# Kernel optimization log

Hardware: AMD Instinct MI355X
Metric: run time of the kernel (lower is better)

The kernel has to match this reference:

```python
import jax, jax.numpy as jnp
import numpy as np

BLOCK = 32          # per_1x32 microscaling block size along K
FP4_MAX = 6.0       # largest magnitude representable in e2m1
FP4_EMAX = 2.0      # exponent of largest fp4 binade (4..6)


def _quant_dequant_mxfp4(x):
    """Simulate MXFP4 (e2m1 elements, shared power-of-two E8M0 scale per 1x32
    block along the last dim): quantize then dequantize. x: [..., K], K % 32 == 0."""
    shape = x.shape
    xb = x.reshape(*shape[:-1], shape[-1] // BLOCK, BLOCK)
    amax = jnp.max(jnp.abs(xb), axis=-1, keepdims=True)
    # shared scale: 2^(floor(log2(amax)) - emax) so the block max lands in the top binade
    exp = jnp.floor(jnp.log2(jnp.maximum(amax, jnp.finfo(x.dtype).tiny))) - FP4_EMAX
    scale = jnp.where(amax > 0, jnp.exp2(exp), jnp.ones_like(amax))
    q = jnp.clip(xb / scale, -FP4_MAX, FP4_MAX)
    aq = jnp.abs(q)
    # e2m1 ulp: 0.5 on [0,2), 1 on [2,4), 2 on [4,6]
    lsb = jnp.where(aq < 2.0, 0.5, jnp.where(aq < 4.0, 1.0, 2.0))
    qr = jnp.round(q / lsb) * lsb  # round-to-nearest-even onto the fp4 grid
    return (qr * scale).reshape(shape)


def setup_inputs() -> dict:
    key = jax.random.key(0)
    k1, k2, k3 = jax.random.split(key, 3)
    B, S, K, N = 4, 2048, 2048, 2048
    inp = jax.random.normal(k1, (B, S, K), dtype=jnp.float32)
    weight = jax.random.normal(k2, (N, K), dtype=jnp.float32) * (1.0 / np.sqrt(K))
    bias = jax.random.normal(k3, (N,), dtype=jnp.float32) * 0.02
    return {"input": inp, "weight": weight, "bias": bias}


def reference(input, weight, bias):
    # both activation and weight are fake-quantized to MXFP4 per 1x32 blocks
    # along the contraction (in_features) dim, then a standard GEMM + bias.
    orig_shape = input.shape
    a = _quant_dequant_mxfp4(input.reshape(-1, orig_shape[-1]))  # [M, K]
    w = _quant_dequant_mxfp4(weight)                              # [N, K]
    out = jnp.einsum("mk,nk->mn", a, w) + bias
    return out.reshape(*orig_shape[:-1], weight.shape[0])
```

## Files before the change

### kernel.cpp

```cpp
#include <hip/hip_runtime.h>
#include <cstdint>


#define BM 128
#define BN 128
#define BK 128
#define NBUF 2

typedef float floatx4 __attribute__((ext_vector_type(4)));
typedef int intx8 __attribute__((ext_vector_type(8)));

#define GLOBAL_AS __attribute__((address_space(1)))
#define LDS_AS __attribute__((address_space(3)))


__device__ __forceinline__ int enc1(float x, float inv) {
    float q = x * inv;
    q = fminf(fmaxf(q, -6.0f), 6.0f);
    int s = (int)(__float_as_uint(q) >> 31) << 3;
    float aq = fabsf(q);
    float ilsb = aq < 2.0f ? 2.0f : (aq < 4.0f ? 1.0f : 0.5f);
    float lsb  = aq < 2.0f ? 0.5f : (aq < 4.0f ? 1.0f : 2.0f);
    float ar = rintf(aq * ilsb) * lsb;
    int c;
    if (ar < 2.0f)      c = (int)(ar * 2.0f);
    else if (ar < 4.0f) c = 2 + (int)ar;
    else                c = 4 + (int)(ar * 0.5f);
    return c | s;
}

__global__ void quant_mxfp4_v3(const float* __restrict__ A, uint8_t* __restrict__ Aq,
                               uint8_t* __restrict__ Asc,
                               const float* __restrict__ W, uint8_t* __restrict__ Wq,
                               uint8_t* __restrict__ Wsc,
                               long na4, long ntot4) {
    long t = (long)blockIdx.x * 256 + threadIdx.x;
    if (t >= ntot4) return;
    const float* src; uint8_t* dq; uint8_t* ds; long idx;
    if (t < na4) { src = A; dq = Aq; ds = Asc; idx = t; }
    else         { src = W; dq = Wq; ds = Wsc; idx = t - na4; }

    float4 f = ((const float4*)src)[idx];
    float amax = fmaxf(fmaxf(fabsf(f.x), fabsf(f.y)),
                       fmaxf(fabsf(f.z), fabsf(f.w)));
    amax = fmaxf(amax, __shfl_xor(amax, 1));
    amax = fmaxf(amax, __shfl_xor(amax, 2));
    amax = fmaxf(amax, __shfl_xor(amax, 4));

    int ebits = (int)((__float_as_uint(amax) >> 23) & 0xff);
    int sb;
    float inv;
    if (amax > 0.0f) {
        sb = ebits - 2; if (sb < 0) sb = 0;
        inv = __uint_as_float((unsigned)((256 - ebits) & 255) << 23);
    } else {
        sb = 127;
        inv = 0.0f;
    }

    int c0 = enc1(f.x, inv), c1 = enc1(f.y, inv);
    int c2 = enc1(f.z, inv), c3 = enc1(f.w, inv);
    ((unsigned short*)dq)[idx] =
        (unsigned short)(c0 | (c1 << 4) | (c2 << 8) | (c3 << 12));
    if ((idx & 7) == 0) ds[idx >> 3] = (uint8_t)sb;
}


__global__ __launch_bounds__(256, 3) void gemm_fp4_pipe(
        const uint8_t* __restrict__ Aq, const uint8_t* __restrict__ Asc,
        const uint8_t* __restrict__ Wq, const uint8_t* __restrict__ Wsc,
        const float* __restrict__ bias, float* __restrict__ C,
        int M, int N, int K) {
    __shared__ __align__(16) uint8_t sA[NBUF][BM * BK / 2];
    __shared__ __align__(16) uint8_t sB[NBUF][BN * BK / 2];
    __shared__ __align__(16) uint8_t sSA[NBUF][BM * 4];
    __shared__ __align__(16) uint8_t sSB[NBUF][BN * 4];

    const int tid = threadIdx.x;
    const int lane = tid & 63;
    const int w = tid >> 6;
    const int wr = w >> 1;
    const int wc = w & 1;
    const int row16 = lane & 15;
    const int quad = lane >> 4;
    const int shq = quad * 8;

    const int id = blockIdx.x;
    const int g = id & 7, h = id >> 3;
    const int by = g + 8 * (h & 7);
    const int bx = h >> 3;
    const int m0 = by * BM;
    const int n0 = bx * BN;
    const int KB2 = K >> 1, KB32 = K >> 5;
    const int NT = K / BK;

    const int fragoff = (quad ^ ((row16 ^ (row16 >> 2)) & 3)) * 16;
    const int rA = wr * 64 + row16;
    const int rB = wc * 64 + row16;

    floatx4 acc[4][4];
#pragma unroll
    for (int i = 0; i < 4; i++)
#pragma unroll
        for (int j = 0; j < 4; j++) acc[i][j] = (floatx4){0.f, 0.f, 0.f, 0.f};

    auto stage = [&](int tt) {
        const int bb = tt & 1;
        const int kb = tt * (BK / 2);
#pragma unroll
        for (int it = 0; it < 2; ++it) {
            int idx = it * 256 + tid;
            int row = idx >> 2, c = idx & 3;
            int gsw = c ^ ((row ^ (row >> 2)) & 3);
            const uint8_t* src = Aq + (size_t)(m0 + row) * KB2 + kb + gsw * 16;
            __builtin_amdgcn_global_load_lds((GLOBAL_AS void*)src,
                (LDS_AS void*)(&sA[bb][idx * 16]), 16, 0, 0);
        }
#pragma unroll
        for (int it = 0; it < 2; ++it) {
            int idx = it * 256 + tid;
            int row = idx >> 2, c = idx & 3;
            int gsw = c ^ ((row ^ (row >> 2)) & 3);
            const uint8_t* src = Wq + (size_t)(n0 + row) * KB2 + kb + gsw * 16;
            __builtin_amdgcn_global_load_lds((GLOBAL_AS void*)src,
                (LDS_AS void*)(&sB[bb][idx * 16]), 16, 0, 0);
        }
        if (tid < 128) {
            const uint8_t* src = Asc + (size_t)(m0 + tid) * KB32 + tt * 4;
            __builtin_amdgcn_global_load_lds((GLOBAL_AS void*)src,
                (LDS_AS void*)(&sSA[bb][tid * 4]), 4, 0, 0);
        } else {
            const uint8_t* src = Wsc + (size_t)(n0 + tid - 128) * KB32 + tt * 4;
            __builtin_amdgcn_global_load_lds((GLOBAL_AS void*)src,
                (LDS_AS void*)(&sSB[bb][(tid - 128) * 4]), 4, 0, 0);
        }
    };

    stage(0);
    if (NT > 1) stage(1);
    if (NT > 1) asm volatile("s_waitcnt vmcnt(5)" ::: "memory");
    else        asm volatile("s_waitcnt vmcnt(0)" ::: "memory");
    __builtin_amdgcn_sched_barrier(0);
    __builtin_amdgcn_s_barrier();
    __builtin_amdgcn_sched_barrier(0);

    for (int t = 0; t < NT; ++t) {
        const int p = t & 1;
        const uint8_t* pa = sA[p];
        const uint8_t* pb = sB[p];

        intx8 A8[4], B8[4];
        int sab[4], swb[4];
#pragma unroll
        for (int ni = 0; ni < 4; ++ni) {
            int r = rB + ni * 16;
            int4 f = *(const int4*)(pb + r * 64 + fragoff);
            B8[ni] = (intx8){f.x, f.y, f.z, f.w, 0, 0, 0, 0};
            swb[ni] = (*(const int*)(&sSB[p][r * 4]) >> shq) & 0xff;
        }
#pragma unroll
        for (int mi = 0; mi < 4; ++mi) {
            int r = rA + mi * 16;
            int4 f = *(const int4*)(pa + r * 64 + fragoff);
            A8[mi] = (intx8){f.x, f.y, f.z, f.w, 0, 0, 0, 0};
            sab[mi] = (*(const int*)(&sSA[p][r * 4]) >> shq) & 0xff;
        }

        asm volatile("s_waitcnt lgkmcnt(0)" ::: "memory");
        __builtin_amdgcn_sched_barrier(0);
        __builtin_amdgcn_s_barrier();
        __builtin_amdgcn_sched_barrier(0);

        if (t + 2 < NT) stage(t + 2);

        __builtin_amdgcn_s_setprio(1);
#pragma unroll
        for (int mi = 0; mi < 4; ++mi) {
#pragma unroll
            for (int ni = 0; ni < 4; ++ni) {
                acc[mi][ni] = __builtin_amdgcn_mfma_scale_f32_16x16x128_f8f6f4(
                    A8[mi], B8[ni], acc[mi][ni], 4, 4, 0, sab[mi], 0, swb[ni]);
            }
        }
        __builtin_amdgcn_s_setprio(0);

        if (t < NT - 1) {
            if (t + 2 < NT) asm volatile("s_waitcnt vmcnt(5)" ::: "memory");
            else            asm volatile("s_waitcnt vmcnt(0)" ::: "memory");
            __builtin_amdgcn_sched_barrier(0);
            __builtin_amdgcn_s_barrier();
            __builtin_amdgcn_sched_barrier(0);
        }
    }

#pragma unroll
    for (int ni = 0; ni < 4; ++ni) {
        int n = n0 + wc * 64 + ni * 16 + row16;
        float bv = bias[n];
#pragma unroll
        for (int mi = 0; mi < 4; ++mi) {
            int mbase = m0 + wr * 64 + mi * 16 + quad * 4;
#pragma unroll
            for (int r = 0; r < 4; ++r) {
                C[(size_t)(mbase + r) * N + n] = acc[mi][ni][r] + bv;
            }
        }
    }
}


extern "C" void kernel_launch(void* const* d_in, const int* in_sizes, int n_in,
                              void* d_out, int out_size, void* d_ws, size_t ws_size,
                              hipStream_t stream) {
    const float* inp  = (const float*)d_in[0];
    const float* wgt  = (const float*)d_in[1];
    const float* bias = (const float*)d_in[2];
    float* out = (float*)d_out;

    const int N = in_sizes[2];
    const int K = in_sizes[1] / N;
    const long M = (long)in_sizes[0] / K;

    uint8_t* Aq4 = (uint8_t*)d_ws;
    uint8_t* Wq4 = Aq4 + (size_t)M * K / 2;
    uint8_t* Asc = Wq4 + (size_t)N * K / 2;
    uint8_t* Wsc = Asc + (size_t)M * K / 32;

    long na4   = (long)M * K / 4;
    long ntot4 = na4 + (long)N * K / 4;
    quant_mxfp4_v3<<<dim3((ntot4 + 255) / 256), dim3(256), 0, stream>>>(
        inp, Aq4, Asc, wgt, Wq4, Wsc, na4, ntot4);

    dim3 grid((N / BN) * (int)(M / BM));
    gemm_fp4_pipe<<<grid, dim3(256), 0, stream>>>(
        Aq4, Asc, Wq4, Wsc, bias, out, (int)M, N, K);
}
```

Before: 160.2 us.

## Transpose MX scale layout, drop LDS swizzle, raise occupancy to 4 waves

```diff
diff --git a/kernel.cpp b/kernel.cpp
--- a/kernel.cpp
+++ b/kernel.cpp
@@ -5,7 +5,6 @@
 #define BM 128
 #define BN 128
 #define BK 128
-#define NBUF 2
 
 typedef float floatx4 __attribute__((ext_vector_type(4)));
 typedef int intx8 __attribute__((ext_vector_type(8)));
@@ -29,16 +28,16 @@
     return c | s;
 }
 
-__global__ void quant_mxfp4_v3(const float* __restrict__ A, uint8_t* __restrict__ Aq,
-                               uint8_t* __restrict__ Asc,
+__global__ void quant_mxfp4_v4(const float* __restrict__ A, uint8_t* __restrict__ Aq,
+                               uint8_t* __restrict__ AscT,
                                const float* __restrict__ W, uint8_t* __restrict__ Wq,
-                               uint8_t* __restrict__ Wsc,
-                               long na4, long ntot4) {
+                               uint8_t* __restrict__ WscT,
+                               long na4, long ntot4, int s4, long Mr, long Nr) {
     long t = (long)blockIdx.x * 256 + threadIdx.x;
     if (t >= ntot4) return;
-    const float* src; uint8_t* dq; uint8_t* ds; long idx;
-    if (t < na4) { src = A; dq = Aq; ds = Asc; idx = t; }
-    else         { src = W; dq = Wq; ds = Wsc; idx = t - na4; }
+    const float* src; uint8_t* dq; uint8_t* ds; long idx; long rows;
+    if (t < na4) { src = A; dq = Aq; ds = AscT; idx = t; rows = Mr; }
+    else         { src = W; dq = Wq; ds = WscT; idx = t - na4; rows = Nr; }
 
     float4 f = ((const float4*)src)[idx];
     float amax = fmaxf(fmaxf(fabsf(f.x), fabsf(f.y)),
@@ -62,19 +61,23 @@
     int c2 = enc1(f.z, inv), c3 = enc1(f.w, inv);
     ((unsigned short*)dq)[idx] =
         (unsigned short)(c0 | (c1 << 4) | (c2 << 8) | (c3 << 12));
-    if ((idx & 7) == 0) ds[idx >> 3] = (uint8_t)sb;
-}
-
-
-__global__ __launch_bounds__(256, 3) void gemm_fp4_pipe(
-        const uint8_t* __restrict__ Aq, const uint8_t* __restrict__ Asc,
-        const uint8_t* __restrict__ Wq, const uint8_t* __restrict__ Wsc,
+    if ((idx & 7) == 0) {
+        long m  = idx >> s4;
+        int  kb = (int)((idx & ((1L << s4) - 1)) >> 3);
+        ds[(size_t)kb * rows + m] = (uint8_t)sb;
+    }
+}
+
+
+__global__ __launch_bounds__(256, 4) void gemm_fp4_v4(
+        const uint8_t* __restrict__ Aq, const uint8_t* __restrict__ AscT,
+        const uint8_t* __restrict__ Wq, const uint8_t* __restrict__ WscT,
         const float* __restrict__ bias, float* __restrict__ C,
         int M, int N, int K) {
-    __shared__ __align__(16) uint8_t sA[NBUF][BM * BK / 2];
-    __shared__ __align__(16) uint8_t sB[NBUF][BN * BK / 2];
-    __shared__ __align__(16) uint8_t sSA[NBUF][BM * 4];
-    __shared__ __align__(16) uint8_t sSB[NBUF][BN * 4];
+    __shared__ __align__(16) uint8_t sA[2][BM * 64];
+    __shared__ __align__(16) uint8_t sB[2][BN * 64];
+    __shared__ __align__(16) uint8_t sSA[2][4 * 128];
+    __shared__ __align__(16) uint8_t sSB[2][4 * 128];
 
     const int tid = threadIdx.x;
     const int lane = tid & 63;
@@ -83,7 +86,6 @@
     const int wc = w & 1;
     const int row16 = lane & 15;
     const int quad = lane >> 4;
-    const int shq = quad * 8;
 
     const int id = blockIdx.x;
     const int g = id & 7, h = id >> 3;
@@ -91,10 +93,9 @@
     const int bx = h >> 3;
     const int m0 = by * BM;
     const int n0 = bx * BN;
-    const int KB2 = K >> 1, KB32 = K >> 5;
+    const int KB2 = K >> 1;
     const int NT = K / BK;
 
-    const int fragoff = (quad ^ ((row16 ^ (row16 >> 2)) & 3)) * 16;
     const int rA = wr * 64 + row16;
     const int rB = wc * 64 + row16;
 
@@ -106,13 +107,12 @@
 
     auto stage = [&](int tt) {
         const int bb = tt & 1;
-        const int kb = tt * (BK / 2);
+        const int kb = tt * 64;
 #pragma unroll
         for (int it = 0; it < 2; ++it) {
             int idx = it * 256 + tid;
             int row = idx >> 2, c = idx & 3;
-            int gsw = c ^ ((row ^ (row >> 2)) & 3);
-            const uint8_t* src = Aq + (size_t)(m0 + row) * KB2 + kb + gsw * 16;
+            const uint8_t* src = Aq + (size_t)(m0 + row) * KB2 + kb + c * 16;
             __builtin_amdgcn_global_load_lds((GLOBAL_AS void*)src,
                 (LDS_AS void*)(&sA[bb][idx * 16]), 16, 0, 0);
         }
@@ -120,66 +120,65 @@
         for (int it = 0; it < 2; ++it) {
             int idx = it * 256 + tid;
             int row = idx >> 2, c = idx & 3;
-            int gsw = c ^ ((row ^ (row >> 2)) & 3);
-            const uint8_t* src = Wq + (size_t)(n0 + row) * KB2 + kb + gsw * 16;
+            const uint8_t* src = Wq + (size_t)(n0 + row) * KB2 + kb + c * 16;
             __builtin_amdgcn_global_load_lds((GLOBAL_AS void*)src,
                 (LDS_AS void*)(&sB[bb][idx * 16]), 16, 0, 0);
         }
         if (tid < 128) {
-            const uint8_t* src = Asc + (size_t)(m0 + tid) * KB32 + tt * 4;
+            int kbi = tid >> 5, moff = (tid & 31) * 4;
+            const uint8_t* src = AscT + (size_t)(4 * tt + kbi) * M + m0 + moff;
             __builtin_amdgcn_global_load_lds((GLOBAL_AS void*)src,
                 (LDS_AS void*)(&sSA[bb][tid * 4]), 4, 0, 0);
         } else {
-            const uint8_t* src = Wsc + (size_t)(n0 + tid - 128) * KB32 + tt * 4;
-            __builtin_amdgcn_global_load_lds((GLOBAL_AS void*)src,
-                (LDS_AS void*)(&sSB[bb][(tid - 128) * 4]), 4, 0, 0);
+            int tw = tid - 128;
+            int kbi = tw >> 5, noff = (tw & 31) * 4;
+            const uint8_t* src = WscT + (size_t)(4 * tt + kbi) * N + n0 + noff;
+            __builtin_amdgcn_global_load_lds((GLOBAL_AS void*)src,
+                (LDS_AS void*)(&sSB[bb][tw * 4]), 4, 0, 0);
         }
     };
 
     stage(0);
-    if (NT > 1) stage(1);
-    if (NT > 1) asm volatile("s_waitcnt vmcnt(5)" ::: "memory");
-    else        asm volatile("s_waitcnt vmcnt(0)" ::: "memory");
+    stage(1);
+    asm volatile("s_waitcnt vmcnt(5)" ::: "memory");
     __builtin_amdgcn_sched_barrier(0);
     __builtin_amdgcn_s_barrier();
-    __builtin_amdgcn_sched_barrier(0);
 
     for (int t = 0; t < NT; ++t) {
         const int p = t & 1;
         const uint8_t* pa = sA[p];
         const uint8_t* pb = sB[p];
 
-        intx8 A8[4], B8[4];
+        int4 afr[4], bfr[4];
         int sab[4], swb[4];
 #pragma unroll
         for (int ni = 0; ni < 4; ++ni) {
             int r = rB + ni * 16;
-            int4 f = *(const int4*)(pb + r * 64 + fragoff);
-            B8[ni] = (intx8){f.x, f.y, f.z, f.w, 0, 0, 0, 0};
-            swb[ni] = (*(const int*)(&sSB[p][r * 4]) >> shq) & 0xff;
+            bfr[ni] = *(const int4*)(pb + r * 64 + quad * 16);
+            swb[ni] = (int)sSB[p][quad * 128 + wc * 64 + ni * 16 + row16];
         }
 #pragma unroll
         for (int mi = 0; mi < 4; ++mi) {
             int r = rA + mi * 16;
-            int4 f = *(const int4*)(pa + r * 64 + fragoff);
-            A8[mi] = (intx8){f.x, f.y, f.z, f.w, 0, 0, 0, 0};
-            sab[mi] = (*(const int*)(&sSA[p][r * 4]) >> shq) & 0xff;
+            afr[mi] = *(const int4*)(pa + r * 64 + quad * 16);
+            sab[mi] = (int)sSA[p][quad * 128 + wr * 64 + mi * 16 + row16];
         }
 
         asm volatile("s_waitcnt lgkmcnt(0)" ::: "memory");
         __builtin_amdgcn_sched_barrier(0);
         __builtin_amdgcn_s_barrier();
-        __builtin_amdgcn_sched_barrier(0);
 
         if (t + 2 < NT) stage(t + 2);
 
         __builtin_amdgcn_s_setprio(1);
 #pragma unroll
         for (int mi = 0; mi < 4; ++mi) {
+            intx8 a8 = {afr[mi].x, afr[mi].y, afr[mi].z, afr[mi].w, 0, 0, 0, 0};
 #pragma unroll
             for (int ni = 0; ni < 4; ++ni) {
+                intx8 b8 = {bfr[ni].x, bfr[ni].y, bfr[ni].z, bfr[ni].w, 0, 0, 0, 0};
                 acc[mi][ni] = __builtin_amdgcn_mfma_scale_f32_16x16x128_f8f6f4(
-                    A8[mi], B8[ni], acc[mi][ni], 4, 4, 0, sab[mi], 0, swb[ni]);
+                    a8, b8, acc[mi][ni], 4, 4, 0, sab[mi], 0, swb[ni]);
             }
         }
         __builtin_amdgcn_s_setprio(0);
@@ -189,7 +188,6 @@
             else            asm volatile("s_waitcnt vmcnt(0)" ::: "memory");
             __builtin_amdgcn_sched_barrier(0);
             __builtin_amdgcn_s_barrier();
-            __builtin_amdgcn_sched_barrier(0);
         }
     }
 
@@ -221,17 +219,20 @@
     const int K = in_sizes[1] / N;
     const long M = (long)in_sizes[0] / K;
 
-    uint8_t* Aq4 = (uint8_t*)d_ws;
-    uint8_t* Wq4 = Aq4 + (size_t)M * K / 2;
-    uint8_t* Asc = Wq4 + (size_t)N * K / 2;
-    uint8_t* Wsc = Asc + (size_t)M * K / 32;
+    uint8_t* Aq4  = (uint8_t*)d_ws;
+    uint8_t* Wq4  = Aq4 + (size_t)M * K / 2;
+    uint8_t* AscT = Wq4 + (size_t)N * K / 2;
+    uint8_t* WscT = AscT + (size_t)M * K / 32;
+
+    int s4 = 0;
+    while ((1 << s4) < (K >> 2)) ++s4;
 
     long na4   = (long)M * K / 4;
     long ntot4 = na4 + (long)N * K / 4;
-    quant_mxfp4_v3<<<dim3((ntot4 + 255) / 256), dim3(256), 0, stream>>>(
-        inp, Aq4, Asc, wgt, Wq4, Wsc, na4, ntot4);
+    quant_mxfp4_v4<<<dim3((ntot4 + 255) / 256), dim3(256), 0, stream>>>(
+        inp, Aq4, AscT, wgt, Wq4, WscT, na4, ntot4, s4, M, (long)N);
 
     dim3 grid((N / BN) * (int)(M / BM));
-    gemm_fp4_pipe<<<grid, dim3(256), 0, stream>>>(
-        Aq4, Asc, Wq4, Wsc, bias, out, (int)M, N, K);
-}
+    gemm_fp4_v4<<<grid, dim3(256), 0, stream>>>(
+        Aq4, AscT, Wq4, WscT, bias, out, (int)M, N, K);
+}
```

New measurement: 156.7 us. 1.02x faster.
